# Performance work log

Hardware: AMD Instinct MI355X
Metric: run time of the kernel (lower is better)

Reference implementation:

```python
import jax, jax.numpy as jnp
import numpy as np
from jax import lax

# --- dims (match init_kwargs / mambapy defaults) ---
D_MODEL = 128
D_STATE = 64
D_CONV = 4
EXPAND = 2
ED = EXPAND * D_MODEL          # 256, d_inner
DT_RANK = (D_MODEL + 15) // 16 # 8, mambapy 'auto'
B_SZ, T = 4, 1024
EPS = 1e-5


def setup_inputs() -> dict:
    key = jax.random.key(0)
    ks = jax.random.split(key, 16)
    s = 0.02
    return {
        "z_seq": jax.random.normal(ks[0], (B_SZ, T, D_MODEL), jnp.float32),
        "aux_tensor": jax.random.normal(ks[1], (B_SZ, T, 3), jnp.float32),
        # wrapper params
        "aux_W": jax.random.normal(ks[2], (D_MODEL, 3), jnp.float32) * s,
        "aux_b": jnp.zeros((D_MODEL,), jnp.float32),
        "ln_w": jnp.ones((D_MODEL,), jnp.float32),
        "ln_b": jnp.zeros((D_MODEL,), jnp.float32),
        # mambapy ResidualBlock RMSNorm
        "rms_w": jnp.ones((D_MODEL,), jnp.float32),
        # MambaBlock params
        "in_proj_W": jax.random.normal(ks[3], (2 * ED, D_MODEL), jnp.float32) * s,
        "conv_W": jax.random.normal(ks[4], (ED, 1, D_CONV), jnp.float32) * s,  # depthwise (O,I/g,K)
        "conv_b": jnp.zeros((ED,), jnp.float32),
        "x_proj_W": jax.random.normal(ks[5], (DT_RANK + 2 * D_STATE, ED), jnp.float32) * s,
        "dt_W": jax.random.normal(ks[6], (ED, DT_RANK), jnp.float32) * s,
        "dt_b": jax.random.uniform(ks[7], (ED,), jnp.float32, -4.0, -2.0),  # softplus -> small dt
        "A_log": jnp.log(jnp.broadcast_to(jnp.arange(1, D_STATE + 1, dtype=jnp.float32), (ED, D_STATE))),
        "D_param": jnp.ones((ED,), jnp.float32),
        "out_proj_W": jax.random.normal(ks[8], (D_MODEL, ED), jnp.float32) * s,
    }


def _mamba_block(x, conv_W, conv_b, in_proj_W, x_proj_W, dt_W, dt_b, A_log, D_param, out_proj_W):
    # x: (B,T,D_MODEL) -> (B,T,D_MODEL)
    xz = x @ in_proj_W.T                             # (B,T,2*ED)
    xs, zg = xz[..., :ED], xz[..., ED:]
    # causal depthwise conv1d over time
    xc = lax.conv_general_dilated(
        xs.transpose(0, 2, 1), conv_W, (1,), ((D_CONV - 1, 0),),
        feature_group_count=ED, dimension_numbers=("NCH", "OIH", "NCH"))
    xs = jax.nn.silu((xc + conv_b[None, :, None]).transpose(0, 2, 1))  # (B,T,ED)
    dbc = xs @ x_proj_W.T                            # (B,T,DT_RANK+2N)
    delta = jax.nn.softplus(dbc[..., :DT_RANK] @ dt_W.T + dt_b)  # (B,T,ED)
    Bm = dbc[..., DT_RANK:DT_RANK + D_STATE]          # (B,T,N)
    Cm = dbc[..., DT_RANK + D_STATE:]                 # (B,T,N)
    A = -jnp.exp(A_log)                               # (ED,N)
    deltaA = jnp.exp(delta[..., None] * A)            # (B,T,ED,N)
    BX = (delta * xs)[..., None] * Bm[:, :, None, :]  # (B,T,ED,N)

    def combine(e1, e2):
        a1, b1 = e1
        a2, b2 = e2
        return a2 * a1, a2 * b1 + b2

    _, h = lax.associative_scan(combine, (deltaA, BX), axis=1)  # h: (B,T,ED,N)
    y = jnp.einsum("bten,btn->bte", h, Cm) + D_param * xs
    y = y * jax.nn.silu(zg)
    return y @ out_proj_W.T


def reference(z_seq, aux_tensor, aux_W, aux_b, ln_w, ln_b, rms_w,
              in_proj_W, conv_W, conv_b, x_proj_W, dt_W, dt_b, A_log, D_param, out_proj_W):
    # wrapper: aux injection
    z = z_seq + aux_tensor @ aux_W.T + aux_b         # (B,T,D)
    # mambapy ResidualBlock: mixer(RMSNorm(z)) + z
    zn = z * lax.rsqrt(jnp.mean(z * z, -1, keepdims=True) + EPS) * rms_w
    core = _mamba_block(zn, conv_W, conv_b, in_proj_W, x_proj_W, dt_W, dt_b,
                        A_log, D_param, out_proj_W) + z
    # wrapper LayerNorm(core + z)
    r = core + z
    mu = jnp.mean(r, -1, keepdims=True)
    var = jnp.mean((r - mu) ** 2, -1, keepdims=True)
    out = (r - mu) * lax.rsqrt(var + EPS) * ln_w + ln_b
    return out
```

## Files before the change

kernel.cpp:

```cpp
#include <hip/hip_runtime.h>
#include <hip/hip_bf16.h>

#define B_SZ 4
#define T_SEQ 1024
#define DM 128
#define ED_ 256
#define NS 64
#define LOG2E 1.44269504088896340736f

#define OFF_Z      0u
#define OFF_ZG     524288u
#define OFF_XSR    1572864u
#define OFF_WC     2621440u
#define OFF_YR     2719744u
#define OFF_DPX    3768320u
#define OFF_BC     5865472u

__device__ __forceinline__ float sigmoidf_(float x){ return 1.f/(1.f+__expf(-x)); }
__device__ __forceinline__ float exp2_(float x){ return __builtin_amdgcn_exp2f(x); }
__device__ __forceinline__ float rlane_(float v, int l){
  return __int_as_float(__builtin_amdgcn_readlane(__float_as_int(v), l));
}
__device__ __forceinline__ void collect_(int &accI, float pp, int t){
  int s;
  asm("v_readlane_b32 %0, %1, 63" : "=s"(s) : "v"(__float_as_int(pp)));
  asm("v_writelane_b32 %0, %1, %2" : "+v"(accI) : "s"(s), "i"(t));
}

#define DPPR(p, ctl) asm("v_add_f32_dpp %0, %0, %0 " ctl " row_mask:0xf bank_mask:0xf bound_ctrl:0" : "+v"(p))
#define DPP6(p) do{ DPPR(p,"row_shr:1"); DPPR(p,"row_shr:2"); DPPR(p,"row_shr:4"); \
                    DPPR(p,"row_shr:8"); DPPR(p,"row_bcast:15"); DPPR(p,"row_bcast:31"); }while(0)

__global__ __launch_bounds__(256) void k0_t(const float* W, float* WTi){
  int k = blockIdx.x;
  int c = threadIdx.x;
  WTi[k*512 + c]       = W[(size_t)c*128 + k];
  WTi[k*512 + c + 256] = W[(size_t)(c+256)*128 + k];
}

__global__ __launch_bounds__(256) void k2_fused(const float* zseq, const float* aux, const float* auxW,
                                                const float* auxb, const float* rmsw, const float* WTi,
                                                const float* xprojW, const float* dtW,
                                                float* z, float* xsr, float* zg, float* WcT){
  if (blockIdx.x >= 512){
    int r = blockIdx.x - 512; int k = threadIdx.x;
    float v;
    if (r < 256){
      v = 0.f;
      #pragma unroll
      for (int j=0;j<8;j++) v += dtW[r*8+j] * xprojW[j*256+k];
    } else {
      v = xprojW[(8 + r-256)*256 + k];
    }
    WcT[k*384 + r] = v;
    return;
  }
  __shared__ float at[128][8];
  int bt0 = blockIdx.x*8; int tid = threadIdx.x;
  {
    int r = tid>>5, l = tid&31;
    int bt = bt0 + r;
    float a0 = aux[bt*3+0], a1 = aux[bt*3+1], a2 = aux[bt*3+2];
    float zv[4]; float ssq = 0.f;
    #pragma unroll
    for (int j=0;j<4;j++){
      int d = l + 32*j;
      float v = zseq[bt*DM+d] + a0*auxW[d*3+0] + a1*auxW[d*3+1] + a2*auxW[d*3+2] + auxb[d];
      zv[j] = v; ssq += v*v;
    }
    #pragma unroll
    for (int m=16;m>=1;m>>=1) ssq += __shfl_xor(ssq, m);
    float rinv = rsqrtf(ssq*(1.f/DM) + 1e-5f);
    #pragma unroll
    for (int j=0;j<4;j++){
      int d = l + 32*j;
      z[bt*DM+d] = zv[j];
      at[d][r] = zv[j]*rinv*rmsw[d];
    }
  }
  __syncthreads();
  float acc0[8], acc1[8];
  #pragma unroll
  for (int r=0;r<8;r++){ acc0[r]=0.f; acc1[r]=0.f; }
  int c0 = tid;
  for (int k=0;k<128;k++){
    float w0 = WTi[k*512 + c0];
    float w1 = WTi[k*512 + c0 + 256];
    float a[8];
    *(float4*)&a[0] = *(const float4*)&at[k][0];
    *(float4*)&a[4] = *(const float4*)&at[k][4];
    #pragma unroll
    for (int r=0;r<8;r++){ acc0[r] = fmaf(a[r], w0, acc0[r]); acc1[r] = fmaf(a[r], w1, acc1[r]); }
  }
  #pragma unroll
  for (int r=0;r<8;r++){
    int bt = bt0+r;
    xsr[bt*ED_ + c0] = acc0[r];
    zg [bt*ED_ + c0] = acc1[r];
  }
}

__global__ __launch_bounds__(384) void k4b_xproj(const float* xsr, const float* convW, const float* convb,
                                                 const float* WcT, const float* dtb,
                                                 float* dxp, float* bcf){
  __shared__ float at[256][8];
  int bt0 = blockIdx.x*8; int tid = threadIdx.x;
  for (int i=tid;i<2048;i+=384){
    int r=i>>8,k=i&255; int bt=bt0+r; int t = bt & (T_SEQ-1);
    float4 wv = *(const float4*)(convW + k*4);
    float s = convb[k];
    if (t>=3) s += xsr[(bt-3)*ED_+k]*wv.x;
    if (t>=2) s += xsr[(bt-2)*ED_+k]*wv.y;
    if (t>=1) s += xsr[(bt-1)*ED_+k]*wv.z;
    s += xsr[bt*ED_+k]*wv.w;
    at[k][r] = s * sigmoidf_(s);
  }
  __syncthreads();
  float acc[8];
  #pragma unroll
  for (int r=0;r<8;r++) acc[r]=0.f;
  int c = tid;
  for (int k=0;k<256;k++){
    float w = WcT[k*384 + c];
    float a[8];
    *(float4*)&a[0] = *(const float4*)&at[k][0];
    *(float4*)&a[4] = *(const float4*)&at[k][4];
    #pragma unroll
    for (int r=0;r<8;r++) acc[r] = fmaf(a[r], w, acc[r]);
  }
  int b4 = bt0 >> 10, tb = bt0 & (T_SEQ-1);
  if (c < 256){
    float bcv = dtb[c];
    float2* pout = (float2*)dxp + (size_t)(b4*ED_ + c)*T_SEQ + tb;
    #pragma unroll
    for (int r=0;r<8;r++){
      float xv = acc[r] + bcv;
      float dv = (xv > 20.f) ? xv : log1pf(__expf(xv));
      pout[r] = make_float2(dv, dv * at[c][r]);
    }
  } else if (c < 320){
    #pragma unroll
    for (int r=0;r<8;r++) bcf[((size_t)(bt0+r)*NS + (c-256))*2 + 0] = acc[r];
  } else {
    #pragma unroll
    for (int r=0;r<8;r++) bcf[((size_t)(bt0+r)*NS + (c-320))*2 + 1] = acc[r];
  }
}

__global__ __launch_bounds__(256,4) void k5_scan(const float* dxpf, const float* bcf,
                                                  const float* Alog, float* yrT,
                                                  const float* outW, float* wot){
  if (blockIdx.x >= 1024){
    int bb = blockIdx.x - 1024;
    int k  = bb*8 + (threadIdx.x>>5);
    int d  = (threadIdx.x&31)*4;
    float4 v;
    v.x = outW[(d+0)*256 + k];
    v.y = outW[(d+1)*256 + k];
    v.z = outW[(d+2)*256 + k];
    v.w = outW[(d+3)*256 + k];
    *(float4*)&wot[k*128 + d] = v;
    return;
  }
  __shared__ float lcar[3][64], lapr[3][64];
  int i = blockIdx.x;
  int w = threadIdx.x >> 6;
  int n = threadIdx.x & 63;
  int x = i & 7;
  int r = i >> 3;
  int b = r & 3;
  int g = r >> 2;
  int e = x*32 + g;
  const int CH = T_SEQ/4;
  int t0 = w*CH;
  float A2 = -__expf(Alog[e*NS+n]) * LOG2E;
  const float2* pd  = (const float2*)dxpf + (size_t)(b*ED_ + e)*T_SEQ + t0;
  const float2* pbc = (const float2*)bcf  + (size_t)(b*T_SEQ + t0)*NS + n;
  float*        py  = yrT + (size_t)(b*ED_ + e)*T_SEQ + t0;

  if (w < 3){
    float h = 0.f, Ssum = 0.f;
    float2 dxc = pd[n];
    for (int sb=0; sb<CH; sb+=64){
      float2 dxn = dxc;
      if (sb+64 < CH) dxn = pd[sb+64+n];
      float sv = dxc.x;
      DPP6(sv);
      Ssum += rlane_(sv, 63);
      float bA[8], bB[8];
      #pragma unroll
      for (int j=0;j<8;j++) bA[j] = pbc[(sb+j)*NS].x;
      #pragma unroll
      for (int bb=0; bb<64; bb+=16){
        #pragma unroll
        for (int j=0;j<8;j++) bB[j] = pbc[(sb+bb+8+j)*NS].x;
        #pragma unroll
        for (int j=0;j<8;j++){
          float sd = rlane_(dxc.x, bb+j);
          float su = rlane_(dxc.y, bb+j);
          h = fmaf(exp2_(sd*A2), h, su*bA[j]);
        }
        if (bb+16 < 64){
          #pragma unroll
          for (int j=0;j<8;j++) bA[j] = pbc[(sb+bb+16+j)*NS].x;
        }
        #pragma unroll
        for (int j=0;j<8;j++){
          float sd = rlane_(dxc.x, bb+8+j);
          float su = rlane_(dxc.y, bb+8+j);
          h = fmaf(exp2_(sd*A2), h, su*bB[j]);
        }
      }
      dxc = dxn;
    }
    lcar[w][n] = h;
    lapr[w][n] = exp2_(A2*Ssum);
  }
  __syncthreads();

  float h = 0.f;
  if (w >= 1) h = lcar[0][n];
  if (w >= 2) h = fmaf(lapr[1][n], h, lcar[1][n]);
  if (w >= 3) h = fmaf(lapr[2][n], h, lcar[2][n]);

  {
    float2 dxc = pd[n];
    for (int sb=0; sb<CH; sb+=64){
      float2 dxn = dxc;
      if (sb+64 < CH) dxn = pd[sb+64+n];
      int accI = 0;
      float2 cA[8], cB[8];
      #pragma unroll
      for (int j=0;j<8;j++) cA[j] = pbc[(sb+j)*NS];
      #pragma unroll
      for (int bb=0; bb<64; bb+=16){
        #pragma unroll
        for (int j=0;j<8;j++) cB[j] = pbc[(sb+bb+8+j)*NS];
        #pragma unroll
        for (int j=0;j<8;j++){
          float sd = rlane_(dxc.x, bb+j);
          float su = rlane_(dxc.y, bb+j);
          h = fmaf(exp2_(sd*A2), h, su*cA[j].x);
          float pp = h*cA[j].y;
          DPP6(pp);
          collect_(accI, pp, bb+j);
        }
        if (bb+16 < 64){
          #pragma unroll
          for (int j=0;j<8;j++) cA[j] = pbc[(sb+bb+16+j)*NS];
        }
        #pragma unroll
        for (int j=0;j<8;j++){
          float sd = rlane_(dxc.x, bb+8+j);
          float su = rlane_(dxc.y, bb+8+j);
          h = fmaf(exp2_(sd*A2), h, su*cB[j].x);
          float pp = h*cB[j].y;
          DPP6(pp);
          collect_(accI, pp, bb+8+j);
        }
      }
      py[sb+n] = __int_as_float(accI);
      dxc = dxn;
    }
  }
}

__global__ __launch_bounds__(256) void k6_out(const float* yrT, const float* dxpf, const float* zg,
                                               const float* Dp, const float* wot, const float* z,
                                               const float* lnw, const float* lnb, float* out){
  __shared__ float yt[256][8];
  __shared__ float xst[256][8];
  __shared__ float psum[4][4], psq[4][4];
  int bt0 = blockIdx.x*8; int tid = threadIdx.x;
  int b4 = bt0 >> 10, tb = bt0 & (T_SEQ-1);
  int el = tid>>3, tl = tid&7;
  #pragma unroll
  for (int gg=0; gg<8; gg++){
    int ee = el + gg*32;
    size_t base = (size_t)(b4*ED_ + ee)*T_SEQ + tb + tl;
    float2 du = ((const float2*)dxpf)[base];
    yt[ee][tl]  = yrT[base];
    xst[ee][tl] = du.y / du.x;
  }
  __syncthreads();
  for (int i=tid;i<2048;i+=256){
    int rr=i>>8, k=i&255; int bt=bt0+rr;
    float zgv = zg[bt*ED_ + k];
    float yv  = yt[k][rr] + Dp[k]*xst[k][rr];
    yt[k][rr] = yv * zgv * sigmoidf_(zgv);
  }
  __syncthreads();
  int d = tid & 127, gdx = tid>>7;
  float acc[4] = {0.f,0.f,0.f,0.f};
  for (int k=0;k<256;k+=4){
    float w0 = wot[(k+0)*128 + d];
    float w1 = wot[(k+1)*128 + d];
    float w2 = wot[(k+2)*128 + d];
    float w3 = wot[(k+3)*128 + d];
    float4 q0 = *(const float4*)&yt[k+0][gdx*4];
    float4 q1 = *(const float4*)&yt[k+1][gdx*4];
    float4 q2 = *(const float4*)&yt[k+2][gdx*4];
    float4 q3 = *(const float4*)&yt[k+3][gdx*4];
    acc[0] = fmaf(q0.x,w0,acc[0]); acc[1] = fmaf(q0.y,w0,acc[1]);
    acc[2] = fmaf(q0.z,w0,acc[2]); acc[3] = fmaf(q0.w,w0,acc[3]);
    acc[0] = fmaf(q1.x,w1,acc[0]); acc[1] = fmaf(q1.y,w1,acc[1]);
    acc[2] = fmaf(q1.z,w1,acc[2]); acc[3] = fmaf(q1.w,w1,acc[3]);
    acc[0] = fmaf(q2.x,w2,acc[0]); acc[1] = fmaf(q2.y,w2,acc[1]);
    acc[2] = fmaf(q2.z,w2,acc[2]); acc[3] = fmaf(q2.w,w2,acc[3]);
    acc[0] = fmaf(q3.x,w3,acc[0]); acc[1] = fmaf(q3.y,w3,acc[1]);
    acc[2] = fmaf(q3.z,w3,acc[2]); acc[3] = fmaf(q3.w,w3,acc[3]);
  }
  float val[4];
  #pragma unroll
  for (int j=0;j<4;j++){
    int bt = bt0 + gdx*4 + j;
    val[j] = acc[j] + 2.f*z[bt*DM + d];
  }
  int w_id = tid>>6;
  #pragma unroll
  for (int j=0;j<4;j++){
    float s = val[j], q = val[j]*val[j];
    #pragma unroll
    for (int off=32; off>=1; off>>=1){ s += __shfl_down(s, off); q += __shfl_down(q, off); }
    if ((tid&63)==0){ psum[w_id][j]=s; psq[w_id][j]=q; }
  }
  __syncthreads();
  float lw = lnw[d], lb = lnb[d];
  #pragma unroll
  for (int j=0;j<4;j++){
    int bt = bt0 + gdx*4 + j;
    float sum = psum[gdx*2][j] + psum[gdx*2+1][j];
    float sq  = psq [gdx*2][j] + psq [gdx*2+1][j];
    float mu  = sum*(1.f/DM);
    float var = sq*(1.f/DM) - mu*mu;
    float inv = rsqrtf(var + 1e-5f);
    out[bt*DM + d] = (val[j]-mu)*inv*lw + lb;
  }
}

extern "C" void kernel_launch(void* const* d_in, const int* in_sizes, int n_in,
                              void* d_out, int out_size, void* d_ws, size_t ws_size,
                              hipStream_t stream){
  const float* zseq = (const float*)d_in[0];
  const float* aux  = (const float*)d_in[1];
  const float* auxW = (const float*)d_in[2];
  const float* auxb = (const float*)d_in[3];
  const float* lnw  = (const float*)d_in[4];
  const float* lnb  = (const float*)d_in[5];
  const float* rmsw = (const float*)d_in[6];
  const float* inW  = (const float*)d_in[7];
  const float* convW= (const float*)d_in[8];
  const float* convb= (const float*)d_in[9];
  const float* xpW  = (const float*)d_in[10];
  const float* dtW  = (const float*)d_in[11];
  const float* dtb  = (const float*)d_in[12];
  const float* Alog = (const float*)d_in[13];
  const float* Dp   = (const float*)d_in[14];
  const float* outW = (const float*)d_in[15];
  float* out = (float*)d_out;
  float* ws = (float*)d_ws;

  float* z   = ws+OFF_Z;
  float* zg  = ws+OFF_ZG;
  float* xsr = ws+OFF_XSR;
  float* wot = ws+OFF_XSR;
  float* WcT = ws+OFF_WC;
  float* yr  = ws+OFF_YR;
  float* wti = ws+OFF_YR;
  float* dxp = ws+OFF_DPX;
  float* bcp = ws+OFF_BC;

  k0_t     <<<128,256,0,stream>>>(inW, wti);
  k2_fused <<<896,256,0,stream>>>(zseq,aux,auxW,auxb,rmsw,wti,xpW,dtW,z,xsr,zg,WcT);
  k4b_xproj<<<512,384,0,stream>>>(xsr,convW,convb,WcT,dtb,dxp,bcp);
  k5_scan  <<<1056,256,0,stream>>>(dxp,bcp,Alog,yr,outW,wot);
  k6_out   <<<512,256,0,stream>>>(yr,dxp,zg,Dp,wot,z,lnw,lnb,out);
}
```

Baseline: 206.0 us.

## Fuse in-projection, causal conv and x-projection into one kernel with halo recompute

Merges the in-projection kernel and the conv+x-projection kernel into a single kernel. Each block recomputes the three preceding timesteps (halo) of the normalized input and x-branch projection, so the causal conv can be applied from registers. This removes the xsr round trip through global memory and one launch. The weight-prep work moves into a single prep kernel. The cost is redundant halo compute, a serialized second GEMM pass for the B/C columns on half the threads, and more registers and shared memory per block.

```diff
diff --git a/kernel.cpp b/kernel.cpp
--- a/kernel.cpp
+++ b/kernel.cpp
@@ -31,119 +31,151 @@
 #define DPP6(p) do{ DPPR(p,"row_shr:1"); DPPR(p,"row_shr:2"); DPPR(p,"row_shr:4"); \
                     DPPR(p,"row_shr:8"); DPPR(p,"row_bcast:15"); DPPR(p,"row_bcast:31"); }while(0)
 
-__global__ __launch_bounds__(256) void k0_t(const float* W, float* WTi){
-  int k = blockIdx.x;
-  int c = threadIdx.x;
-  WTi[k*512 + c]       = W[(size_t)c*128 + k];
-  WTi[k*512 + c + 256] = W[(size_t)(c+256)*128 + k];
-}
-
-__global__ __launch_bounds__(256) void k2_fused(const float* zseq, const float* aux, const float* auxW,
-                                                const float* auxb, const float* rmsw, const float* WTi,
-                                                const float* xprojW, const float* dtW,
-                                                float* z, float* xsr, float* zg, float* WcT){
-  if (blockIdx.x >= 512){
-    int r = blockIdx.x - 512; int k = threadIdx.x;
-    float v;
-    if (r < 256){
-      v = 0.f;
-      #pragma unroll
-      for (int j=0;j<8;j++) v += dtW[r*8+j] * xprojW[j*256+k];
-    } else {
-      v = xprojW[(8 + r-256)*256 + k];
-    }
-    WcT[k*384 + r] = v;
+__global__ __launch_bounds__(256) void k0_prep(const float* W, const float* xprojW, const float* dtW,
+                                               float* WTi, float* WcT){
+  if (blockIdx.x < 128){
+    int k = blockIdx.x;
+    int c = threadIdx.x;
+    WTi[k*512 + c]       = W[(size_t)c*128 + k];
+    WTi[k*512 + c + 256] = W[(size_t)(c+256)*128 + k];
     return;
   }
-  __shared__ float at[128][8];
+  int r = blockIdx.x - 128; int k = threadIdx.x;
+  float v;
+  if (r < 256){
+    v = 0.f;
+    #pragma unroll
+    for (int j=0;j<8;j++) v += dtW[r*8+j] * xprojW[j*256+k];
+  } else {
+    v = xprojW[(8 + r-256)*256 + k];
+  }
+  WcT[k*384 + r] = v;
+}
+
+__global__ __launch_bounds__(256,4) void k24(const float* zseq, const float* aux, const float* auxW,
+                                             const float* auxb, const float* rmsw, const float* WTi,
+                                             const float* convW, const float* convb,
+                                             const float* WcT, const float* dtb,
+                                             float* z, float* zg, float* dxp, float* bcf){
+  __shared__ float at[128][12];
+  __shared__ float xsl[256][12];
   int bt0 = blockIdx.x*8; int tid = threadIdx.x;
+  int t0 = bt0 & (T_SEQ-1);
+
   {
-    int r = tid>>5, l = tid&31;
-    int bt = bt0 + r;
-    float a0 = aux[bt*3+0], a1 = aux[bt*3+1], a2 = aux[bt*3+2];
-    float zv[4]; float ssq = 0.f;
-    #pragma unroll
-    for (int j=0;j<4;j++){
-      int d = l + 32*j;
-      float v = zseq[bt*DM+d] + a0*auxW[d*3+0] + a1*auxW[d*3+1] + a2*auxW[d*3+2] + auxb[d];
-      zv[j] = v; ssq += v*v;
-    }
-    #pragma unroll
-    for (int m=16;m>=1;m>>=1) ssq += __shfl_xor(ssq, m);
-    float rinv = rsqrtf(ssq*(1.f/DM) + 1e-5f);
-    #pragma unroll
-    for (int j=0;j<4;j++){
-      int d = l + 32*j;
-      z[bt*DM+d] = zv[j];
-      at[d][r] = zv[j]*rinv*rmsw[d];
-    }
-  }
-  __syncthreads();
-  float acc0[8], acc1[8];
-  #pragma unroll
-  for (int r=0;r<8;r++){ acc0[r]=0.f; acc1[r]=0.f; }
+    int l = tid & 31;
+    #pragma unroll
+    for (int pass=0; pass<2; pass++){
+      int h = (pass==0) ? (tid>>5) : (8 + (tid>>5));
+      bool active = (pass==0) || (tid < 96);
+      if (active){
+        int bt = bt0 - 3 + h;
+        if (bt >= 0){
+          float a0 = aux[bt*3+0], a1 = aux[bt*3+1], a2 = aux[bt*3+2];
+          float zv[4]; float ssq = 0.f;
+          #pragma unroll
+          for (int j=0;j<4;j++){
+            int d = l + 32*j;
+            float v = zseq[bt*DM+d] + a0*auxW[d*3+0] + a1*auxW[d*3+1] + a2*auxW[d*3+2] + auxb[d];
+            zv[j] = v; ssq += v*v;
+          }
+          #pragma unroll
+          for (int m=16;m>=1;m>>=1) ssq += __shfl_xor(ssq, m);
+          float rinv = rsqrtf(ssq*(1.f/DM) + 1e-5f);
+          #pragma unroll
+          for (int j=0;j<4;j++){
+            int d = l + 32*j;
+            if (h >= 3) z[bt*DM+d] = zv[j];
+            at[d][h] = zv[j]*rinv*rmsw[d];
+          }
+        } else {
+          #pragma unroll
+          for (int j=0;j<4;j++) at[l+32*j][h] = 0.f;
+        }
+      }
+    }
+  }
+  __syncthreads();
+
+  float acc0[11], acc1[8];
+  #pragma unroll
+  for (int h=0;h<11;h++) acc0[h]=0.f;
+  #pragma unroll
+  for (int r=0;r<8;r++) acc1[r]=0.f;
   int c0 = tid;
   for (int k=0;k<128;k++){
     float w0 = WTi[k*512 + c0];
     float w1 = WTi[k*512 + c0 + 256];
-    float a[8];
+    float a[12];
     *(float4*)&a[0] = *(const float4*)&at[k][0];
     *(float4*)&a[4] = *(const float4*)&at[k][4];
-    #pragma unroll
-    for (int r=0;r<8;r++){ acc0[r] = fmaf(a[r], w0, acc0[r]); acc1[r] = fmaf(a[r], w1, acc1[r]); }
-  }
-  #pragma unroll
-  for (int r=0;r<8;r++){
-    int bt = bt0+r;
-    xsr[bt*ED_ + c0] = acc0[r];
-    zg [bt*ED_ + c0] = acc1[r];
-  }
-}
-
-__global__ __launch_bounds__(384) void k4b_xproj(const float* xsr, const float* convW, const float* convb,
-                                                 const float* WcT, const float* dtb,
-                                                 float* dxp, float* bcf){
-  __shared__ float at[256][8];
-  int bt0 = blockIdx.x*8; int tid = threadIdx.x;
-  for (int i=tid;i<2048;i+=384){
-    int r=i>>8,k=i&255; int bt=bt0+r; int t = bt & (T_SEQ-1);
-    float4 wv = *(const float4*)(convW + k*4);
-    float s = convb[k];
-    if (t>=3) s += xsr[(bt-3)*ED_+k]*wv.x;
-    if (t>=2) s += xsr[(bt-2)*ED_+k]*wv.y;
-    if (t>=1) s += xsr[(bt-1)*ED_+k]*wv.z;
-    s += xsr[bt*ED_+k]*wv.w;
-    at[k][r] = s * sigmoidf_(s);
-  }
-  __syncthreads();
-  float acc[8];
-  #pragma unroll
-  for (int r=0;r<8;r++) acc[r]=0.f;
-  int c = tid;
-  for (int k=0;k<256;k++){
-    float w = WcT[k*384 + c];
-    float a[8];
-    *(float4*)&a[0] = *(const float4*)&at[k][0];
-    *(float4*)&a[4] = *(const float4*)&at[k][4];
-    #pragma unroll
-    for (int r=0;r<8;r++) acc[r] = fmaf(a[r], w, acc[r]);
-  }
-  int b4 = bt0 >> 10, tb = bt0 & (T_SEQ-1);
-  if (c < 256){
+    *(float4*)&a[8] = *(const float4*)&at[k][8];
+    #pragma unroll
+    for (int h=0;h<11;h++) acc0[h] = fmaf(a[h], w0, acc0[h]);
+    #pragma unroll
+    for (int r=0;r<8;r++)  acc1[r] = fmaf(a[3+r], w1, acc1[r]);
+  }
+  #pragma unroll
+  for (int r=0;r<8;r++) zg[(bt0+r)*ED_ + c0] = acc1[r];
+
+  {
+    float4 cw = *(const float4*)(convW + c0*4);
+    float cb = convb[c0];
+    #pragma unroll
+    for (int r=0;r<8;r++){
+      int t = t0 + r;
+      float s = fmaf(acc0[r+3], cw.w, cb);
+      if (t >= 1) s = fmaf(acc0[r+2], cw.z, s);
+      if (t >= 2) s = fmaf(acc0[r+1], cw.y, s);
+      if (t >= 3) s = fmaf(acc0[r+0], cw.x, s);
+      xsl[c0][r] = s * sigmoidf_(s);
+    }
+  }
+  __syncthreads();
+
+  int b4 = bt0 >> 10;
+  {
+    float acc[8];
+    #pragma unroll
+    for (int r=0;r<8;r++) acc[r]=0.f;
+    int c = tid;
+    for (int k=0;k<256;k++){
+      float w = WcT[k*384 + c];
+      float a[8];
+      *(float4*)&a[0] = *(const float4*)&xsl[k][0];
+      *(float4*)&a[4] = *(const float4*)&xsl[k][4];
+      #pragma unroll
+      for (int r=0;r<8;r++) acc[r] = fmaf(a[r], w, acc[r]);
+    }
     float bcv = dtb[c];
-    float2* pout = (float2*)dxp + (size_t)(b4*ED_ + c)*T_SEQ + tb;
+    float2* pout = (float2*)dxp + (size_t)(b4*ED_ + c)*T_SEQ + t0;
     #pragma unroll
     for (int r=0;r<8;r++){
       float xv = acc[r] + bcv;
       float dv = (xv > 20.f) ? xv : log1pf(__expf(xv));
-      pout[r] = make_float2(dv, dv * at[c][r]);
-    }
-  } else if (c < 320){
-    #pragma unroll
-    for (int r=0;r<8;r++) bcf[((size_t)(bt0+r)*NS + (c-256))*2 + 0] = acc[r];
-  } else {
-    #pragma unroll
-    for (int r=0;r<8;r++) bcf[((size_t)(bt0+r)*NS + (c-320))*2 + 1] = acc[r];
+      pout[r] = make_float2(dv, dv * xsl[c][r]);
+    }
+  }
+  if (tid < 128){
+    int c = 256 + tid;
+    float acc[8];
+    #pragma unroll
+    for (int r=0;r<8;r++) acc[r]=0.f;
+    for (int k=0;k<256;k++){
+      float w = WcT[k*384 + c];
+      float a[8];
+      *(float4*)&a[0] = *(const float4*)&xsl[k][0];
+      *(float4*)&a[4] = *(const float4*)&xsl[k][4];
+      #pragma unroll
+      for (int r=0;r<8;r++) acc[r] = fmaf(a[r], w, acc[r]);
+    }
+    if (tid < 64){
+      #pragma unroll
+      for (int r=0;r<8;r++) bcf[((size_t)(bt0+r)*NS + tid)*2 + 0] = acc[r];
+    } else {
+      #pragma unroll
+      for (int r=0;r<8;r++) bcf[((size_t)(bt0+r)*NS + (tid-64))*2 + 1] = acc[r];
+    }
   }
 }
 
@@ -362,7 +394,6 @@
 
   float* z   = ws+OFF_Z;
   float* zg  = ws+OFF_ZG;
-  float* xsr = ws+OFF_XSR;
   float* wot = ws+OFF_XSR;
   float* WcT = ws+OFF_WC;
   float* yr  = ws+OFF_YR;
@@ -370,9 +401,8 @@
   float* dxp = ws+OFF_DPX;
   float* bcp = ws+OFF_BC;
 
-  k0_t     <<<128,256,0,stream>>>(inW, wti);
-  k2_fused <<<896,256,0,stream>>>(zseq,aux,auxW,auxb,rmsw,wti,xpW,dtW,z,xsr,zg,WcT);
-  k4b_xproj<<<512,384,0,stream>>>(xsr,convW,convb,WcT,dtb,dxp,bcp);
-  k5_scan  <<<1056,256,0,stream>>>(dxp,bcp,Alog,yr,outW,wot);
-  k6_out   <<<512,256,0,stream>>>(yr,dxp,zg,Dp,wot,z,lnw,lnb,out);
-}
+  k0_prep <<<512,256,0,stream>>>(inW, xpW, dtW, wti, WcT);
+  k24     <<<512,256,0,stream>>>(zseq,aux,auxW,auxb,rmsw,wti,convW,convb,WcT,dtb,z,zg,dxp,bcp);
+  k5_scan <<<1056,256,0,stream>>>(dxp,bcp,Alog,yr,outW,wot);
+  k6_out  <<<512,256,0,stream>>>(yr,dxp,zg,Dp,wot,z,lnw,lnb,out);
+}
```

Result: slower. 217.0 us (+5.3%).

## Scan two channels per wave and reduce C-products through LDS instead of DPP

Applied to the files above, without the earlier changes.

Each wave in the selective-scan kernel now advances two d_inner channels at once. The B/C loads are shared between them, and the two independent recurrences give the scheduler more instruction-level parallelism. The per-timestep six-step DPP reduction over the state dimension, plus readlane/writelane collection, is replaced by writing the h*C products to LDS. Every 16 steps a transposed LDS read and a cross-half shuffle reduce them. Blocks grow to 512 threads covering four channels, which cuts the grid to a quarter. That lowers the total wave count and may reduce latency hiding, and it adds LDS traffic.

```diff
diff --git a/kernel.cpp b/kernel.cpp
--- a/kernel.cpp
+++ b/kernel.cpp
@@ -20,11 +20,6 @@
 __device__ __forceinline__ float exp2_(float x){ return __builtin_amdgcn_exp2f(x); }
 __device__ __forceinline__ float rlane_(float v, int l){
   return __int_as_float(__builtin_amdgcn_readlane(__float_as_int(v), l));
-}
-__device__ __forceinline__ void collect_(int &accI, float pp, int t){
-  int s;
-  asm("v_readlane_b32 %0, %1, 63" : "=s"(s) : "v"(__float_as_int(pp)));
-  asm("v_writelane_b32 %0, %1, %2" : "+v"(accI) : "s"(s), "i"(t));
 }
 
 #define DPPR(p, ctl) asm("v_add_f32_dpp %0, %0, %0 " ctl " row_mask:0xf bank_mask:0xf bound_ctrl:0" : "+v"(p))
@@ -147,12 +142,12 @@
   }
 }
 
-__global__ __launch_bounds__(256,4) void k5_scan(const float* dxpf, const float* bcf,
+__global__ __launch_bounds__(512,2) void k5_scan(const float* dxpf, const float* bcf,
                                                   const float* Alog, float* yrT,
                                                   const float* outW, float* wot){
-  if (blockIdx.x >= 1024){
-    int bb = blockIdx.x - 1024;
-    int k  = bb*8 + (threadIdx.x>>5);
+  if (blockIdx.x >= 256){
+    int bb2 = blockIdx.x - 256;
+    int k  = bb2*16 + (threadIdx.x>>5);
     int d  = (threadIdx.x&31)*4;
     float4 v;
     v.x = outW[(d+0)*256 + k];
@@ -162,43 +157,52 @@
     *(float4*)&wot[k*128 + d] = v;
     return;
   }
-  __shared__ float lcar[3][64], lapr[3][64];
-  int i = blockIdx.x;
-  int w = threadIdx.x >> 6;
-  int n = threadIdx.x & 63;
+  __shared__ float lcar[3][4][64], lapr[3][4][64];
+  __shared__ float red[8][16][2][66];
+  int i  = blockIdx.x;
+  int tid = threadIdx.x;
+  int wv = tid >> 6;
+  int n  = tid & 63;
+  int w  = wv >> 1;
+  int half = wv & 1;
   int x = i & 7;
   int r = i >> 3;
   int b = r & 3;
   int g = r >> 2;
-  int e = x*32 + g;
+  int eA = x*32 + g*4 + half*2;
+  int eB = eA + 1;
   const int CH = T_SEQ/4;
   int t0 = w*CH;
-  float A2 = -__expf(Alog[e*NS+n]) * LOG2E;
-  const float2* pd  = (const float2*)dxpf + (size_t)(b*ED_ + e)*T_SEQ + t0;
+  float A2A = -__expf(Alog[eA*NS+n]) * LOG2E;
+  float A2B = -__expf(Alog[eB*NS+n]) * LOG2E;
+  const float2* pdA = (const float2*)dxpf + (size_t)(b*ED_ + eA)*T_SEQ + t0;
+  const float2* pdB = (const float2*)dxpf + (size_t)(b*ED_ + eB)*T_SEQ + t0;
   const float2* pbc = (const float2*)bcf  + (size_t)(b*T_SEQ + t0)*NS + n;
-  float*        py  = yrT + (size_t)(b*ED_ + e)*T_SEQ + t0;
-
-  if (w < 3){
-    float h = 0.f, Ssum = 0.f;
-    float2 dxc = pd[n];
+  float* pyA = yrT + (size_t)(b*ED_ + eA)*T_SEQ + t0;
+  float* pyB = yrT + (size_t)(b*ED_ + eB)*T_SEQ + t0;
+  int el = half*2;
+
+  if (wv < 6){
+    float hA=0.f, hB=0.f, SsA=0.f, SsB=0.f;
+    float2 dxcA = pdA[n], dxcB = pdB[n];
     for (int sb=0; sb<CH; sb+=64){
-      float2 dxn = dxc;
-      if (sb+64 < CH) dxn = pd[sb+64+n];
-      float sv = dxc.x;
-      DPP6(sv);
-      Ssum += rlane_(sv, 63);
-      float bA[8], bB[8];
+      float2 dxnA = dxcA, dxnB = dxcB;
+      if (sb+64 < CH){ dxnA = pdA[sb+64+n]; dxnB = pdB[sb+64+n]; }
+      float svA = dxcA.x; DPP6(svA); SsA += rlane_(svA, 63);
+      float svB = dxcB.x; DPP6(svB); SsB += rlane_(svB, 63);
+      float bA[8], bBv[8];
       #pragma unroll
       for (int j=0;j<8;j++) bA[j] = pbc[(sb+j)*NS].x;
       #pragma unroll
       for (int bb=0; bb<64; bb+=16){
         #pragma unroll
-        for (int j=0;j<8;j++) bB[j] = pbc[(sb+bb+8+j)*NS].x;
+        for (int j=0;j<8;j++) bBv[j] = pbc[(sb+bb+8+j)*NS].x;
         #pragma unroll
         for (int j=0;j<8;j++){
-          float sd = rlane_(dxc.x, bb+j);
-          float su = rlane_(dxc.y, bb+j);
-          h = fmaf(exp2_(sd*A2), h, su*bA[j]);
+          float sdA = rlane_(dxcA.x, bb+j), suA = rlane_(dxcA.y, bb+j);
+          hA = fmaf(exp2_(sdA*A2A), hA, suA*bA[j]);
+          float sdB = rlane_(dxcB.x, bb+j), suB = rlane_(dxcB.y, bb+j);
+          hB = fmaf(exp2_(sdB*A2B), hB, suB*bA[j]);
         }
         if (bb+16 < 64){
           #pragma unroll
@@ -206,29 +210,35 @@
         }
         #pragma unroll
         for (int j=0;j<8;j++){
-          float sd = rlane_(dxc.x, bb+8+j);
-          float su = rlane_(dxc.y, bb+8+j);
-          h = fmaf(exp2_(sd*A2), h, su*bB[j]);
+          float sdA = rlane_(dxcA.x, bb+8+j), suA = rlane_(dxcA.y, bb+8+j);
+          hA = fmaf(exp2_(sdA*A2A), hA, suA*bBv[j]);
+          float sdB = rlane_(dxcB.x, bb+8+j), suB = rlane_(dxcB.y, bb+8+j);
+          hB = fmaf(exp2_(sdB*A2B), hB, suB*bBv[j]);
         }
       }
-      dxc = dxn;
-    }
-    lcar[w][n] = h;
-    lapr[w][n] = exp2_(A2*Ssum);
-  }
-  __syncthreads();
-
-  float h = 0.f;
-  if (w >= 1) h = lcar[0][n];
-  if (w >= 2) h = fmaf(lapr[1][n], h, lcar[1][n]);
-  if (w >= 3) h = fmaf(lapr[2][n], h, lcar[2][n]);
+      dxcA = dxnA; dxcB = dxnB;
+    }
+    lcar[w][el  ][n] = hA;  lapr[w][el  ][n] = exp2_(A2A*SsA);
+    lcar[w][el+1][n] = hB;  lapr[w][el+1][n] = exp2_(A2B*SsB);
+  }
+  __syncthreads();
+
+  float hA = 0.f, hB = 0.f;
+  #pragma unroll
+  for (int q=0;q<3;q++) if (w > q){
+    hA = fmaf(lapr[q][el  ][n], hA, lcar[q][el  ][n]);
+    hB = fmaf(lapr[q][el+1][n], hB, lcar[q][el+1][n]);
+  }
 
   {
-    float2 dxc = pd[n];
+    float2 dxcA = pdA[n], dxcB = pdB[n];
+    int ri = n & 31, hs = n >> 5;
+    int eh = ri >> 4, tr = ri & 15;
+    const float2* rp = (const float2*)&red[wv][tr][eh][hs*32];
+    float* pyE = eh ? pyB : pyA;
     for (int sb=0; sb<CH; sb+=64){
-      float2 dxn = dxc;
-      if (sb+64 < CH) dxn = pd[sb+64+n];
-      int accI = 0;
+      float2 dxnA = dxcA, dxnB = dxcB;
+      if (sb+64 < CH){ dxnA = pdA[sb+64+n]; dxnB = pdB[sb+64+n]; }
       float2 cA[8], cB[8];
       #pragma unroll
       for (int j=0;j<8;j++) cA[j] = pbc[(sb+j)*NS];
@@ -238,12 +248,12 @@
         for (int j=0;j<8;j++) cB[j] = pbc[(sb+bb+8+j)*NS];
         #pragma unroll
         for (int j=0;j<8;j++){
-          float sd = rlane_(dxc.x, bb+j);
-          float su = rlane_(dxc.y, bb+j);
-          h = fmaf(exp2_(sd*A2), h, su*cA[j].x);
-          float pp = h*cA[j].y;
-          DPP6(pp);
-          collect_(accI, pp, bb+j);
+          float sdA = rlane_(dxcA.x, bb+j), suA = rlane_(dxcA.y, bb+j);
+          hA = fmaf(exp2_(sdA*A2A), hA, suA*cA[j].x);
+          red[wv][j][0][n] = hA*cA[j].y;
+          float sdB = rlane_(dxcB.x, bb+j), suB = rlane_(dxcB.y, bb+j);
+          hB = fmaf(exp2_(sdB*A2B), hB, suB*cA[j].x);
+          red[wv][j][1][n] = hB*cA[j].y;
         }
         if (bb+16 < 64){
           #pragma unroll
@@ -251,16 +261,20 @@
         }
         #pragma unroll
         for (int j=0;j<8;j++){
-          float sd = rlane_(dxc.x, bb+8+j);
-          float su = rlane_(dxc.y, bb+8+j);
-          h = fmaf(exp2_(sd*A2), h, su*cB[j].x);
-          float pp = h*cB[j].y;
-          DPP6(pp);
-          collect_(accI, pp, bb+8+j);
-        }
+          float sdA = rlane_(dxcA.x, bb+8+j), suA = rlane_(dxcA.y, bb+8+j);
+          hA = fmaf(exp2_(sdA*A2A), hA, suA*cB[j].x);
+          red[wv][8+j][0][n] = hA*cB[j].y;
+          float sdB = rlane_(dxcB.x, bb+8+j), suB = rlane_(dxcB.y, bb+8+j);
+          hB = fmaf(exp2_(sdB*A2B), hB, suB*cB[j].x);
+          red[wv][8+j][1][n] = hB*cB[j].y;
+        }
+        float s = 0.f;
+        #pragma unroll
+        for (int jj=0;jj<16;jj++){ float2 v = rp[jj]; s += v.x + v.y; }
+        s += __shfl_xor(s, 32);
+        if (n < 32) pyE[sb + bb + tr] = s;
       }
-      py[sb+n] = __int_as_float(accI);
-      dxc = dxn;
+      dxcA = dxnA; dxcB = dxnB;
     }
   }
 }
@@ -373,6 +387,6 @@
   k0_t     <<<128,256,0,stream>>>(inW, wti);
   k2_fused <<<896,256,0,stream>>>(zseq,aux,auxW,auxb,rmsw,wti,xpW,dtW,z,xsr,zg,WcT);
   k4b_xproj<<<512,384,0,stream>>>(xsr,convW,convb,WcT,dtb,dxp,bcp);
-  k5_scan  <<<1056,256,0,stream>>>(dxp,bcp,Alog,yr,outW,wot);
+  k5_scan  <<<272,512,0,stream>>>(dxp,bcp,Alog,yr,outW,wot);
   k6_out   <<<512,256,0,stream>>>(yr,dxp,zg,Dp,wot,z,lnw,lnb,out);
 }
```

Result: faster. 187.2 us (-9.2%).
